# Kernel optimization log

Hardware: AMD Instinct MI355X
Metric: run time of the kernel (lower is better)

The kernel has to match this reference:

```python
import jax, jax.numpy as jnp
import numpy as np

N_NODES = 100000
N_EDGES = 3200000
OUT_CH = 128
X_DIM = 128


def setup_inputs() -> dict:
    key = jax.random.key(0)
    k1, k2, k3, k4 = jax.random.split(key, 4)
    x = jax.random.normal(k1, (N_NODES, X_DIM), dtype=jnp.float32)
    edge_index = jax.random.randint(k2, (2, N_EDGES), 0, N_NODES, dtype=jnp.int64)
    # torch nn.Linear(num_nodes, out_channels): weight [out, N], bias [out]
    W_weight = jax.random.normal(k3, (OUT_CH, N_NODES), dtype=jnp.float32) * (1.0 / np.sqrt(N_NODES))
    W_bias = jax.random.normal(k4, (OUT_CH,), dtype=jnp.float32) * 0.01
    return {"x": x, "edge_index": edge_index, "W_weight": W_weight, "W_bias": W_bias}


def reference(x, edge_index, W_weight, W_bias):
    """LINK forward: logits = A @ W.T + b, A = sparse COO adjacency from edge_index.

    A[r, c] = 1 for each edge (r, c), so row r of the output is
    sum_{c in neighbors(r)} W.T[c] + b  -> gather + segment_sum (SpMM).
    """
    N = x.shape[0]
    row, col = edge_index[0], edge_index[1]
    Wt = W_weight.T  # [N, out]
    gathered = Wt[col]  # [E, out] irregular gather
    logits = jax.ops.segment_sum(gathered, row, num_segments=N) + W_bias  # [N, out]
    return logits
```

## Files before the change

kernel.cpp:

```cpp
#include <hip/hip_runtime.h>
#include <hip/hip_bf16.h>


#define NCHUNK 256
#define RPB 64
#define MAXBUCK 1600
#define CAP 3072
#define SCAN_CHUNK 256

__global__ __launch_bounds__(256) void absmax_kernel(const float* __restrict__ W,
                                                     int n4,
                                                     unsigned int* __restrict__ amax) {
    int i = blockIdx.x * blockDim.x + threadIdx.x;
    int stride = gridDim.x * blockDim.x;
    float m = 0.f;
    const float4* W4 = (const float4*)W;
    for (; i < n4; i += stride) {
        float4 v = W4[i];
        m = fmaxf(m, fmaxf(fmaxf(fabsf(v.x), fabsf(v.y)),
                           fmaxf(fabsf(v.z), fabsf(v.w))));
    }
    for (int off = 32; off > 0; off >>= 1) m = fmaxf(m, __shfl_xor(m, off));
    if ((threadIdx.x & 63) == 0)
        atomicMax(amax, __float_as_uint(m));
}

__global__ __launch_bounds__(256) void quant_kernel(const float* __restrict__ W,
                                                    unsigned char* __restrict__ Wt8,
                                                    const unsigned int* __restrict__ amax,
                                                    int N) {
    __shared__ float tile[128][33];
    int cx = threadIdx.x;
    int oy = threadIdx.y;
    int c = blockIdx.x * 32 + cx;
    for (int k = 0; k < 16; ++k) {
        int o = oy * 16 + k;
        tile[o][cx] = (c < N) ? W[(size_t)o * N + c] : 0.f;
    }
    __syncthreads();
    float M = __uint_as_float(*amax);
    float si = (M > 0.f) ? 127.f / M : 0.f;
    if (c < N) {
        unsigned int w[4];
#pragma unroll
        for (int d = 0; d < 4; ++d) {
            unsigned int acc = 0;
#pragma unroll
            for (int b = 0; b < 4; ++b) {
                int o = oy * 16 + d * 4 + b;
                int qi = __float2int_rn(tile[o][cx] * si) + 128;
                acc |= ((unsigned int)(qi & 0xff)) << (8 * b);
            }
            w[d] = acc;
        }
        *(uint4*)(Wt8 + (size_t)c * 128 + oy * 16) =
            make_uint4(w[0], w[1], w[2], w[3]);
    }
}

__global__ __launch_bounds__(256) void p1_hist(const int* __restrict__ row,
                                               int E, int nbuck,
                                               int* __restrict__ hist) {
    __shared__ int lh[MAXBUCK];
    int b = blockIdx.x;
    for (int k = threadIdx.x; k < nbuck; k += blockDim.x) lh[k] = 0;
    __syncthreads();
    int ch = (E + NCHUNK - 1) / NCHUNK;
    int s = b * ch, e = min(E, s + ch);
    for (int i = s + threadIdx.x; i < e; i += blockDim.x)
        atomicAdd(&lh[row[i] >> 6], 1);
    __syncthreads();
    for (int k = threadIdx.x; k < nbuck; k += blockDim.x)
        hist[k * NCHUNK + b] = lh[k];
}

__global__ void scan_sums(const int* __restrict__ v, int* __restrict__ bsums,
                          int M) {
    __shared__ int s[SCAN_CHUNK];
    int i = blockIdx.x * SCAN_CHUNK + threadIdx.x;
    s[threadIdx.x] = (i < M) ? v[i] : 0;
    __syncthreads();
    for (int off = SCAN_CHUNK / 2; off > 0; off >>= 1) {
        if (threadIdx.x < off) s[threadIdx.x] += s[threadIdx.x + off];
        __syncthreads();
    }
    if (threadIdx.x == 0) bsums[blockIdx.x] = s[0];
}

__global__ __launch_bounds__(256) void scan_offsets_par(int* __restrict__ bsums,
                                                        int nb) {
    __shared__ int s[256];
    __shared__ int carry;
    if (threadIdx.x == 0) carry = 0;
    __syncthreads();
    for (int base = 0; base < nb; base += 256) {
        int i = base + threadIdx.x;
        int v = (i < nb) ? bsums[i] : 0;
        s[threadIdx.x] = v;
        __syncthreads();
        for (int off = 1; off < 256; off <<= 1) {
            int t = (threadIdx.x >= off) ? s[threadIdx.x - off] : 0;
            __syncthreads();
            s[threadIdx.x] += t;
            __syncthreads();
        }
        int incl = s[threadIdx.x];
        int c = carry;
        __syncthreads();
        if (threadIdx.x == 255) carry = c + incl;
        if (i < nb) bsums[i] = c + incl - v;
        __syncthreads();
    }
}

__global__ void scan_final(const int* __restrict__ v,
                           const int* __restrict__ bsums,
                           int* __restrict__ S, int M) {
    __shared__ int s[SCAN_CHUNK];
    int i = blockIdx.x * SCAN_CHUNK + threadIdx.x;
    int x = (i < M) ? v[i] : 0;
    s[threadIdx.x] = x;
    __syncthreads();
    for (int off = 1; off < SCAN_CHUNK; off <<= 1) {
        int t = (threadIdx.x >= off) ? s[threadIdx.x - off] : 0;
        __syncthreads();
        s[threadIdx.x] += t;
        __syncthreads();
    }
    if (i < M) S[i] = bsums[blockIdx.x] + s[threadIdx.x] - x;
}

__global__ __launch_bounds__(256) void p1_scatter(const int* __restrict__ row,
                                                  const int* __restrict__ col,
                                                  int E, int nbuck,
                                                  const int* __restrict__ S,
                                                  unsigned* __restrict__ packed) {
    __shared__ int lc[MAXBUCK];
    int b = blockIdx.x;
    for (int k = threadIdx.x; k < nbuck; k += blockDim.x)
        lc[k] = S[k * NCHUNK + b];
    __syncthreads();
    int ch = (E + NCHUNK - 1) / NCHUNK;
    int s = b * ch, e = min(E, s + ch);
    for (int i = s + threadIdx.x; i < e; i += blockDim.x) {
        int r = row[i], c = col[i];
        int p = atomicAdd(&lc[r >> 6], 1);
        packed[p] = ((unsigned)(r & 63) << 26) | ((unsigned)c << 7);
    }
}

__global__ __launch_bounds__(256) void spmm_fused(
    const unsigned* __restrict__ packed, const int* __restrict__ S,
    const unsigned char* __restrict__ Wt8, const float* __restrict__ bias,
    const unsigned int* __restrict__ amax, float* __restrict__ out, int E,
    int N, int nbuck) {
    __shared__ unsigned g2[CAP];
    __shared__ int rhist[RPB];
    __shared__ int rowstart[RPB + 1];
    __shared__ int cursor[RPB];
    int k = blockIdx.x;
    int start = S[k * NCHUNK];
    int end = (k + 1 < nbuck) ? S[(k + 1) * NCHUNK] : E;
    int cnt = end - start;
    if (cnt > CAP) cnt = CAP;
    if (threadIdx.x < RPB) rhist[threadIdx.x] = 0;
    __syncthreads();
    for (int i = threadIdx.x; i < cnt; i += blockDim.x)
        atomicAdd(&rhist[packed[start + i] >> 26], 1);
    __syncthreads();
    if (threadIdx.x == 0) {
        int acc = 0;
        for (int r = 0; r < RPB; ++r) { rowstart[r] = acc; acc += rhist[r]; }
        rowstart[RPB] = acc;
    }
    __syncthreads();
    if (threadIdx.x < RPB) cursor[threadIdx.x] = rowstart[threadIdx.x];
    __syncthreads();
    for (int i = threadIdx.x; i < cnt; i += blockDim.x) {
        unsigned e2 = packed[start + i];
        int p = atomicAdd(&cursor[e2 >> 26], 1);
        g2[p] = e2 & 0x03FFFFFFu;
    }
    __syncthreads();

    float sg = __uint_as_float(*amax) / 127.f;
    int wave = threadIdx.x >> 6, lane = threadIdx.x & 63;
    int h = lane >> 5;
    int lane4 = (lane & 31) * 4;

    for (int r = wave; r < RPB; r += 4) {
        int gr = k * RPB + r;
        if (gr >= N) break;
        int js = rowstart[r], je = rowstart[r + 1];
        int m = je - js;
        int T = m >> 1;
        unsigned accA = 0, accB = 0;
        int idx = js + h;
        int t = 0;
        for (; t + 4 <= T; t += 4) {
            unsigned e0 = g2[idx + 0];
            unsigned e1 = g2[idx + 2];
            unsigned e2 = g2[idx + 4];
            unsigned e3 = g2[idx + 6];
            idx += 8;
            uint32_t u0 = *(const uint32_t*)(Wt8 + e0 + lane4);
            uint32_t u1 = *(const uint32_t*)(Wt8 + e1 + lane4);
            uint32_t u2 = *(const uint32_t*)(Wt8 + e2 + lane4);
            uint32_t u3 = *(const uint32_t*)(Wt8 + e3 + lane4);
            accA += (u0 & 0x00FF00FFu);
            accB += ((u0 >> 8) & 0x00FF00FFu);
            accA += (u1 & 0x00FF00FFu);
            accB += ((u1 >> 8) & 0x00FF00FFu);
            accA += (u2 & 0x00FF00FFu);
            accB += ((u2 >> 8) & 0x00FF00FFu);
            accA += (u3 & 0x00FF00FFu);
            accB += ((u3 >> 8) & 0x00FF00FFu);
        }
        for (; t < T; ++t) {
            unsigned e0 = g2[idx];
            idx += 2;
            uint32_t u0 = *(const uint32_t*)(Wt8 + e0 + lane4);
            accA += (u0 & 0x00FF00FFu);
            accB += ((u0 >> 8) & 0x00FF00FFu);
        }
        if ((m & 1) && h == 0) {
            unsigned e0 = g2[je - 1];
            uint32_t u0 = *(const uint32_t*)(Wt8 + e0 + lane4);
            accA += (u0 & 0x00FF00FFu);
            accB += ((u0 >> 8) & 0x00FF00FFu);
        }
        accA += __shfl_xor(accA, 32);
        accB += __shfl_xor(accB, 32);
        if (h == 0) {
            float fm = -128.f * (float)m;
            float4 b4 = *(const float4*)(bias + lane4);
            float4 res;
            res.x = fmaf(sg, (float)(accA & 0xffffu) + fm, b4.x);
            res.y = fmaf(sg, (float)(accB & 0xffffu) + fm, b4.y);
            res.z = fmaf(sg, (float)(accA >> 16) + fm, b4.z);
            res.w = fmaf(sg, (float)(accB >> 16) + fm, b4.w);
            *(float4*)(out + (size_t)gr * 128 + lane4) = res;
        }
    }
}

extern "C" void kernel_launch(void* const* d_in, const int* in_sizes, int n_in,
                              void* d_out, int out_size, void* d_ws,
                              size_t ws_size, hipStream_t stream) {
    const int* edge = (const int*)d_in[1];
    const float* W = (const float*)d_in[2];
    const float* bias = (const float*)d_in[3];
    float* out = (float*)d_out;

    const int N = in_sizes[0] / 128;
    const int E = in_sizes[1] / 2;
    const int* row = edge;
    const int* col = edge + E;

    const int nbuck = (N + RPB - 1) / RPB;
    const int M = nbuck * NCHUNK;
    const int nb = (M + SCAN_CHUNK - 1) / SCAN_CHUNK;

    auto align16 = [](size_t v) { return (v + 15) & ~(size_t)15; };
    char* ws = (char*)d_ws;
    size_t off = 0;
    unsigned char* Wt8 = (unsigned char*)(ws + off);
    off = align16(off + (size_t)N * 128);
    unsigned* packed = (unsigned*)(ws + off);
    off = align16(off + (size_t)E * sizeof(unsigned));
    int* hist = (int*)(ws + off);
    off = align16(off + (size_t)M * sizeof(int));
    int* S = (int*)(ws + off);
    off = align16(off + (size_t)M * sizeof(int));
    int* bsums = (int*)(ws + off);
    off = align16(off + (size_t)nb * sizeof(int));
    unsigned int* amax = (unsigned int*)(ws + off);
    off = align16(off + 16);

    hipMemsetAsync(amax, 0, sizeof(unsigned int), stream);

    absmax_kernel<<<1024, 256, 0, stream>>>(W, (128 * N) / 4, amax);
    {
        dim3 block(32, 8);
        dim3 grid((N + 31) / 32);
        quant_kernel<<<grid, block, 0, stream>>>(W, Wt8, amax, N);
    }
    p1_hist<<<NCHUNK, 256, 0, stream>>>(row, E, nbuck, hist);
    scan_sums<<<nb, SCAN_CHUNK, 0, stream>>>(hist, bsums, M);
    scan_offsets_par<<<1, 256, 0, stream>>>(bsums, nb);
    scan_final<<<nb, SCAN_CHUNK, 0, stream>>>(hist, bsums, S, M);
    p1_scatter<<<NCHUNK, 256, 0, stream>>>(row, col, E, nbuck, S, packed);
    spmm_fused<<<nbuck, 256, 0, stream>>>(packed, S, Wt8, bias, amax, out, E, N,
                                          nbuck);
}
```

Baseline: 205.7 us.

## Quadruple bucketing chunks, transpose scan offsets, and use 8-byte gathers in SpMM

Raises the number of histogram/scatter chunks from 256 to 1024 so more blocks run the bucketing phase in parallel. The scan becomes two-level to handle the larger offset array, and it writes a transposed offset table plus a compact per-bucket start array. This makes offset loads coalesced in the scatter and gives the SpMM a direct lookup. The SpMM now splits each wave into four quarter-groups, each loading 8 bytes per edge, with an extra shuffle stage to combine them. The cost is extra scan kernel launches and a hist/offset array four times larger.

```diff
diff --git a/kernel.cpp b/kernel.cpp
--- a/kernel.cpp
+++ b/kernel.cpp
@@ -2,11 +2,10 @@
 #include <hip/hip_bf16.h>
 
 
-#define NCHUNK 256
+#define NCHUNK 1024
 #define RPB 64
 #define MAXBUCK 1600
 #define CAP 3072
-#define SCAN_CHUNK 256
 
 __global__ __launch_bounds__(256) void absmax_kernel(const float* __restrict__ W,
                                                      int n4,
@@ -74,13 +73,13 @@
         hist[k * NCHUNK + b] = lh[k];
 }
 
-__global__ void scan_sums(const int* __restrict__ v, int* __restrict__ bsums,
-                          int M) {
-    __shared__ int s[SCAN_CHUNK];
-    int i = blockIdx.x * SCAN_CHUNK + threadIdx.x;
+__global__ __launch_bounds__(256) void scan_sums(const int* __restrict__ v,
+                                                 int* __restrict__ bsums, int M) {
+    __shared__ int s[256];
+    int i = blockIdx.x * 256 + threadIdx.x;
     s[threadIdx.x] = (i < M) ? v[i] : 0;
     __syncthreads();
-    for (int off = SCAN_CHUNK / 2; off > 0; off >>= 1) {
+    for (int off = 128; off > 0; off >>= 1) {
         if (threadIdx.x < off) s[threadIdx.x] += s[threadIdx.x + off];
         __syncthreads();
     }
@@ -113,32 +112,57 @@
     }
 }
 
-__global__ void scan_final(const int* __restrict__ v,
-                           const int* __restrict__ bsums,
-                           int* __restrict__ S, int M) {
-    __shared__ int s[SCAN_CHUNK];
-    int i = blockIdx.x * SCAN_CHUNK + threadIdx.x;
+__global__ __launch_bounds__(256) void scan_final_inplace(int* __restrict__ v,
+                                                          const int* __restrict__ bsums,
+                                                          int M) {
+    __shared__ int s[256];
+    int i = blockIdx.x * 256 + threadIdx.x;
     int x = (i < M) ? v[i] : 0;
     s[threadIdx.x] = x;
     __syncthreads();
-    for (int off = 1; off < SCAN_CHUNK; off <<= 1) {
+    for (int off = 1; off < 256; off <<= 1) {
         int t = (threadIdx.x >= off) ? s[threadIdx.x - off] : 0;
         __syncthreads();
         s[threadIdx.x] += t;
         __syncthreads();
     }
-    if (i < M) S[i] = bsums[blockIdx.x] + s[threadIdx.x] - x;
+    if (i < M) v[i] = bsums[blockIdx.x] + s[threadIdx.x] - x;
+}
+
+__global__ __launch_bounds__(256) void scan_finalT(const int* __restrict__ hist,
+                                                   const int* __restrict__ bsums,
+                                                   int* __restrict__ S_T,
+                                                   int* __restrict__ bstart,
+                                                   int M, int nbuck) {
+    __shared__ int s[256];
+    int i = blockIdx.x * 256 + threadIdx.x;
+    int x = (i < M) ? hist[i] : 0;
+    s[threadIdx.x] = x;
+    __syncthreads();
+    for (int off = 1; off < 256; off <<= 1) {
+        int t = (threadIdx.x >= off) ? s[threadIdx.x - off] : 0;
+        __syncthreads();
+        s[threadIdx.x] += t;
+        __syncthreads();
+    }
+    if (i < M) {
+        int val = bsums[blockIdx.x] + s[threadIdx.x] - x;
+        int k = i >> 10;
+        int b = i & (NCHUNK - 1);
+        S_T[(size_t)b * nbuck + k] = val;
+        if (b == 0) bstart[k] = val;
+    }
 }
 
 __global__ __launch_bounds__(256) void p1_scatter(const int* __restrict__ row,
                                                   const int* __restrict__ col,
                                                   int E, int nbuck,
-                                                  const int* __restrict__ S,
+                                                  const int* __restrict__ S_T,
                                                   unsigned* __restrict__ packed) {
     __shared__ int lc[MAXBUCK];
     int b = blockIdx.x;
-    for (int k = threadIdx.x; k < nbuck; k += blockDim.x)
-        lc[k] = S[k * NCHUNK + b];
+    const int* Srow = S_T + (size_t)b * nbuck;
+    for (int k = threadIdx.x; k < nbuck; k += blockDim.x) lc[k] = Srow[k];
     __syncthreads();
     int ch = (E + NCHUNK - 1) / NCHUNK;
     int s = b * ch, e = min(E, s + ch);
@@ -150,7 +174,7 @@
 }
 
 __global__ __launch_bounds__(256) void spmm_fused(
-    const unsigned* __restrict__ packed, const int* __restrict__ S,
+    const unsigned* __restrict__ packed, const int* __restrict__ bstart,
     const unsigned char* __restrict__ Wt8, const float* __restrict__ bias,
     const unsigned int* __restrict__ amax, float* __restrict__ out, int E,
     int N, int nbuck) {
@@ -159,8 +183,8 @@
     __shared__ int rowstart[RPB + 1];
     __shared__ int cursor[RPB];
     int k = blockIdx.x;
-    int start = S[k * NCHUNK];
-    int end = (k + 1 < nbuck) ? S[(k + 1) * NCHUNK] : E;
+    int start = bstart[k];
+    int end = (k + 1 < nbuck) ? bstart[k + 1] : E;
     int cnt = end - start;
     if (cnt > CAP) cnt = CAP;
     if (threadIdx.x < RPB) rhist[threadIdx.x] = 0;
@@ -185,61 +209,72 @@
 
     float sg = __uint_as_float(*amax) / 127.f;
     int wave = threadIdx.x >> 6, lane = threadIdx.x & 63;
-    int h = lane >> 5;
-    int lane4 = (lane & 31) * 4;
+    int q = lane >> 4;
+    int sl8 = (lane & 15) * 8;
 
     for (int r = wave; r < RPB; r += 4) {
         int gr = k * RPB + r;
         if (gr >= N) break;
         int js = rowstart[r], je = rowstart[r + 1];
         int m = je - js;
-        int T = m >> 1;
-        unsigned accA = 0, accB = 0;
-        int idx = js + h;
+        unsigned aA0 = 0, aB0 = 0, aA1 = 0, aB1 = 0;
+        int nq = m >> 2;
+        int base = js + q;
         int t = 0;
-        for (; t + 4 <= T; t += 4) {
-            unsigned e0 = g2[idx + 0];
-            unsigned e1 = g2[idx + 2];
-            unsigned e2 = g2[idx + 4];
-            unsigned e3 = g2[idx + 6];
-            idx += 8;
-            uint32_t u0 = *(const uint32_t*)(Wt8 + e0 + lane4);
-            uint32_t u1 = *(const uint32_t*)(Wt8 + e1 + lane4);
-            uint32_t u2 = *(const uint32_t*)(Wt8 + e2 + lane4);
-            uint32_t u3 = *(const uint32_t*)(Wt8 + e3 + lane4);
-            accA += (u0 & 0x00FF00FFu);
-            accB += ((u0 >> 8) & 0x00FF00FFu);
-            accA += (u1 & 0x00FF00FFu);
-            accB += ((u1 >> 8) & 0x00FF00FFu);
-            accA += (u2 & 0x00FF00FFu);
-            accB += ((u2 >> 8) & 0x00FF00FFu);
-            accA += (u3 & 0x00FF00FFu);
-            accB += ((u3 >> 8) & 0x00FF00FFu);
-        }
-        for (; t < T; ++t) {
-            unsigned e0 = g2[idx];
-            idx += 2;
-            uint32_t u0 = *(const uint32_t*)(Wt8 + e0 + lane4);
-            accA += (u0 & 0x00FF00FFu);
-            accB += ((u0 >> 8) & 0x00FF00FFu);
-        }
-        if ((m & 1) && h == 0) {
-            unsigned e0 = g2[je - 1];
-            uint32_t u0 = *(const uint32_t*)(Wt8 + e0 + lane4);
-            accA += (u0 & 0x00FF00FFu);
-            accB += ((u0 >> 8) & 0x00FF00FFu);
-        }
-        accA += __shfl_xor(accA, 32);
-        accB += __shfl_xor(accB, 32);
-        if (h == 0) {
+        for (; t + 2 <= nq; t += 2) {
+            unsigned e0 = g2[base + 4 * t];
+            unsigned e1 = g2[base + 4 * t + 4];
+            uint2 u0 = *(const uint2*)(Wt8 + e0 + sl8);
+            uint2 u1 = *(const uint2*)(Wt8 + e1 + sl8);
+            aA0 += u0.x & 0x00FF00FFu;
+            aB0 += (u0.x >> 8) & 0x00FF00FFu;
+            aA1 += u0.y & 0x00FF00FFu;
+            aB1 += (u0.y >> 8) & 0x00FF00FFu;
+            aA0 += u1.x & 0x00FF00FFu;
+            aB0 += (u1.x >> 8) & 0x00FF00FFu;
+            aA1 += u1.y & 0x00FF00FFu;
+            aB1 += (u1.y >> 8) & 0x00FF00FFu;
+        }
+        if (t < nq) {
+            unsigned e0 = g2[base + 4 * t];
+            uint2 u0 = *(const uint2*)(Wt8 + e0 + sl8);
+            aA0 += u0.x & 0x00FF00FFu;
+            aB0 += (u0.x >> 8) & 0x00FF00FFu;
+            aA1 += u0.y & 0x00FF00FFu;
+            aB1 += (u0.y >> 8) & 0x00FF00FFu;
+        }
+        int rem = m & 3;
+        if (q < rem) {
+            unsigned e0 = g2[js + (nq << 2) + q];
+            uint2 u0 = *(const uint2*)(Wt8 + e0 + sl8);
+            aA0 += u0.x & 0x00FF00FFu;
+            aB0 += (u0.x >> 8) & 0x00FF00FFu;
+            aA1 += u0.y & 0x00FF00FFu;
+            aB1 += (u0.y >> 8) & 0x00FF00FFu;
+        }
+        aA0 += __shfl_xor(aA0, 16);
+        aB0 += __shfl_xor(aB0, 16);
+        aA1 += __shfl_xor(aA1, 16);
+        aB1 += __shfl_xor(aB1, 16);
+        aA0 += __shfl_xor(aA0, 32);
+        aB0 += __shfl_xor(aB0, 32);
+        aA1 += __shfl_xor(aA1, 32);
+        aB1 += __shfl_xor(aB1, 32);
+        if (q == 0) {
             float fm = -128.f * (float)m;
-            float4 b4 = *(const float4*)(bias + lane4);
-            float4 res;
-            res.x = fmaf(sg, (float)(accA & 0xffffu) + fm, b4.x);
-            res.y = fmaf(sg, (float)(accB & 0xffffu) + fm, b4.y);
-            res.z = fmaf(sg, (float)(accA >> 16) + fm, b4.z);
-            res.w = fmaf(sg, (float)(accB >> 16) + fm, b4.w);
-            *(float4*)(out + (size_t)gr * 128 + lane4) = res;
+            float4 b0 = *(const float4*)(bias + sl8);
+            float4 b1 = *(const float4*)(bias + sl8 + 4);
+            float4 r0, r1;
+            r0.x = fmaf(sg, (float)(aA0 & 0xffffu) + fm, b0.x);
+            r0.y = fmaf(sg, (float)(aB0 & 0xffffu) + fm, b0.y);
+            r0.z = fmaf(sg, (float)(aA0 >> 16) + fm, b0.z);
+            r0.w = fmaf(sg, (float)(aB0 >> 16) + fm, b0.w);
+            r1.x = fmaf(sg, (float)(aA1 & 0xffffu) + fm, b1.x);
+            r1.y = fmaf(sg, (float)(aB1 & 0xffffu) + fm, b1.y);
+            r1.z = fmaf(sg, (float)(aA1 >> 16) + fm, b1.z);
+            r1.w = fmaf(sg, (float)(aB1 >> 16) + fm, b1.w);
+            *(float4*)(out + (size_t)gr * 128 + sl8) = r0;
+            *(float4*)(out + (size_t)gr * 128 + sl8 + 4) = r1;
         }
     }
 }
@@ -259,7 +294,8 @@
 
     const int nbuck = (N + RPB - 1) / RPB;
     const int M = nbuck * NCHUNK;
-    const int nb = (M + SCAN_CHUNK - 1) / SCAN_CHUNK;
+    const int nb1 = (M + 255) / 256;
+    const int nb2 = (nb1 + 255) / 256;
 
     auto align16 = [](size_t v) { return (v + 15) & ~(size_t)15; };
     char* ws = (char*)d_ws;
@@ -270,10 +306,14 @@
     off = align16(off + (size_t)E * sizeof(unsigned));
     int* hist = (int*)(ws + off);
     off = align16(off + (size_t)M * sizeof(int));
-    int* S = (int*)(ws + off);
+    int* S_T = (int*)(ws + off);
     off = align16(off + (size_t)M * sizeof(int));
-    int* bsums = (int*)(ws + off);
-    off = align16(off + (size_t)nb * sizeof(int));
+    int* bs1 = (int*)(ws + off);
+    off = align16(off + (size_t)nb1 * sizeof(int));
+    int* bs2 = (int*)(ws + off);
+    off = align16(off + (size_t)nb2 * sizeof(int));
+    int* bstart = (int*)(ws + off);
+    off = align16(off + (size_t)(nbuck + 1) * sizeof(int));
     unsigned int* amax = (unsigned int*)(ws + off);
     off = align16(off + 16);
 
@@ -286,10 +326,12 @@
         quant_kernel<<<grid, block, 0, stream>>>(W, Wt8, amax, N);
     }
     p1_hist<<<NCHUNK, 256, 0, stream>>>(row, E, nbuck, hist);
-    scan_sums<<<nb, SCAN_CHUNK, 0, stream>>>(hist, bsums, M);
-    scan_offsets_par<<<1, 256, 0, stream>>>(bsums, nb);
-    scan_final<<<nb, SCAN_CHUNK, 0, stream>>>(hist, bsums, S, M);
-    p1_scatter<<<NCHUNK, 256, 0, stream>>>(row, col, E, nbuck, S, packed);
-    spmm_fused<<<nbuck, 256, 0, stream>>>(packed, S, Wt8, bias, amax, out, E, N,
-                                          nbuck);
-}
+    scan_sums<<<nb1, 256, 0, stream>>>(hist, bs1, M);
+    scan_sums<<<nb2, 256, 0, stream>>>(bs1, bs2, nb1);
+    scan_offsets_par<<<1, 256, 0, stream>>>(bs2, nb2);
+    scan_final_inplace<<<nb2, 256, 0, stream>>>(bs1, bs2, nb1);
+    scan_finalT<<<nb1, 256, 0, stream>>>(hist, bs1, S_T, bstart, M, nbuck);
+    p1_scatter<<<NCHUNK, 256, 0, stream>>>(row, col, E, nbuck, S_T, packed);
+    spmm_fused<<<nbuck, 256, 0, stream>>>(packed, bstart, Wt8, bias, amax, out,
+                                          E, N, nbuck);
+}
```

After: 230.1 us. 1.12x slower.

## Widen buckets to 128 rows, use 1024-thread blocks, transpose scan offsets

Applied to the files above, without the earlier changes.

Doubles rows per bucket to 128 (782 buckets, fixed as a compile-time constant) and runs the hist, scatter and SpMM kernels with 1024 threads. Scan offsets are written transposed so each scatter block reads a contiguous row, and a separate bucket-start array is emitted. The SpMM kernel keeps edges in registers between the histogram and placement passes, so packed is read only once, and replaces the serial row scan with a parallel scan. The packed format now stores the column directly and shifts it at placement. The hardcoded NB7 ties the code to N=100000. The CAP of 5120 silently drops edges if a bucket ever exceeds it.

```diff
diff --git a/kernel.cpp b/kernel.cpp
--- a/kernel.cpp
+++ b/kernel.cpp
@@ -3,10 +3,9 @@
 
 
 #define NCHUNK 256
-#define RPB 64
-#define MAXBUCK 1600
-#define CAP 3072
-#define SCAN_CHUNK 256
+#define RPB7 128
+#define NB7 782
+#define CAP 5120
 
 __global__ __launch_bounds__(256) void absmax_kernel(const float* __restrict__ W,
                                                      int n4,
@@ -21,8 +20,7 @@
                            fmaxf(fabsf(v.z), fabsf(v.w))));
     }
     for (int off = 32; off > 0; off >>= 1) m = fmaxf(m, __shfl_xor(m, off));
-    if ((threadIdx.x & 63) == 0)
-        atomicMax(amax, __float_as_uint(m));
+    if ((threadIdx.x & 63) == 0) atomicMax(amax, __float_as_uint(m));
 }
 
 __global__ __launch_bounds__(256) void quant_kernel(const float* __restrict__ W,
@@ -58,29 +56,28 @@
     }
 }
 
-__global__ __launch_bounds__(256) void p1_hist(const int* __restrict__ row,
-                                               int E, int nbuck,
-                                               int* __restrict__ hist) {
-    __shared__ int lh[MAXBUCK];
+__global__ __launch_bounds__(1024) void p1_hist(const int* __restrict__ row,
+                                                int E, int* __restrict__ hist) {
+    __shared__ int lh[NB7];
     int b = blockIdx.x;
-    for (int k = threadIdx.x; k < nbuck; k += blockDim.x) lh[k] = 0;
+    for (int k = threadIdx.x; k < NB7; k += blockDim.x) lh[k] = 0;
     __syncthreads();
     int ch = (E + NCHUNK - 1) / NCHUNK;
     int s = b * ch, e = min(E, s + ch);
     for (int i = s + threadIdx.x; i < e; i += blockDim.x)
-        atomicAdd(&lh[row[i] >> 6], 1);
-    __syncthreads();
-    for (int k = threadIdx.x; k < nbuck; k += blockDim.x)
+        atomicAdd(&lh[row[i] >> 7], 1);
+    __syncthreads();
+    for (int k = threadIdx.x; k < NB7; k += blockDim.x)
         hist[k * NCHUNK + b] = lh[k];
 }
 
-__global__ void scan_sums(const int* __restrict__ v, int* __restrict__ bsums,
-                          int M) {
-    __shared__ int s[SCAN_CHUNK];
-    int i = blockIdx.x * SCAN_CHUNK + threadIdx.x;
+__global__ __launch_bounds__(256) void scan_sums(const int* __restrict__ v,
+                                                 int* __restrict__ bsums, int M) {
+    __shared__ int s[256];
+    int i = blockIdx.x * 256 + threadIdx.x;
     s[threadIdx.x] = (i < M) ? v[i] : 0;
     __syncthreads();
-    for (int off = SCAN_CHUNK / 2; off > 0; off >>= 1) {
+    for (int off = 128; off > 0; off >>= 1) {
         if (threadIdx.x < off) s[threadIdx.x] += s[threadIdx.x + off];
         __syncthreads();
     }
@@ -113,85 +110,127 @@
     }
 }
 
-__global__ void scan_final(const int* __restrict__ v,
-                           const int* __restrict__ bsums,
-                           int* __restrict__ S, int M) {
-    __shared__ int s[SCAN_CHUNK];
-    int i = blockIdx.x * SCAN_CHUNK + threadIdx.x;
-    int x = (i < M) ? v[i] : 0;
+__global__ __launch_bounds__(256) void scan_finalT(const int* __restrict__ hist,
+                                                   const int* __restrict__ bsums,
+                                                   int* __restrict__ S_T,
+                                                   int* __restrict__ bstart,
+                                                   int M) {
+    __shared__ int s[256];
+    int i = blockIdx.x * 256 + threadIdx.x;
+    int x = (i < M) ? hist[i] : 0;
     s[threadIdx.x] = x;
     __syncthreads();
-    for (int off = 1; off < SCAN_CHUNK; off <<= 1) {
+    for (int off = 1; off < 256; off <<= 1) {
         int t = (threadIdx.x >= off) ? s[threadIdx.x - off] : 0;
         __syncthreads();
         s[threadIdx.x] += t;
         __syncthreads();
     }
-    if (i < M) S[i] = bsums[blockIdx.x] + s[threadIdx.x] - x;
-}
-
-__global__ __launch_bounds__(256) void p1_scatter(const int* __restrict__ row,
-                                                  const int* __restrict__ col,
-                                                  int E, int nbuck,
-                                                  const int* __restrict__ S,
-                                                  unsigned* __restrict__ packed) {
-    __shared__ int lc[MAXBUCK];
+    if (i < M) {
+        int val = bsums[blockIdx.x] + s[threadIdx.x] - x;
+        int k = i >> 8;
+        int b = i & (NCHUNK - 1);
+        S_T[(size_t)b * NB7 + k] = val;
+        if (b == 0) bstart[k] = val;
+    }
+}
+
+__global__ __launch_bounds__(1024) void p1_scatter(const int* __restrict__ row,
+                                                   const int* __restrict__ col,
+                                                   int E,
+                                                   const int* __restrict__ S_T,
+                                                   unsigned* __restrict__ packed) {
+    __shared__ int lc[NB7];
     int b = blockIdx.x;
-    for (int k = threadIdx.x; k < nbuck; k += blockDim.x)
-        lc[k] = S[k * NCHUNK + b];
+    const int* Srow = S_T + (size_t)b * NB7;
+    for (int k = threadIdx.x; k < NB7; k += blockDim.x) lc[k] = Srow[k];
     __syncthreads();
     int ch = (E + NCHUNK - 1) / NCHUNK;
     int s = b * ch, e = min(E, s + ch);
     for (int i = s + threadIdx.x; i < e; i += blockDim.x) {
         int r = row[i], c = col[i];
-        int p = atomicAdd(&lc[r >> 6], 1);
-        packed[p] = ((unsigned)(r & 63) << 26) | ((unsigned)c << 7);
-    }
-}
-
-__global__ __launch_bounds__(256) void spmm_fused(
-    const unsigned* __restrict__ packed, const int* __restrict__ S,
+        int p = atomicAdd(&lc[r >> 7], 1);
+        packed[p] = ((unsigned)(r & 127) << 17) | (unsigned)c;
+    }
+}
+
+__global__ __launch_bounds__(1024) void spmm_fused(
+    const unsigned* __restrict__ packed, const int* __restrict__ bstart,
     const unsigned char* __restrict__ Wt8, const float* __restrict__ bias,
     const unsigned int* __restrict__ amax, float* __restrict__ out, int E,
-    int N, int nbuck) {
+    int N) {
     __shared__ unsigned g2[CAP];
-    __shared__ int rhist[RPB];
-    __shared__ int rowstart[RPB + 1];
-    __shared__ int cursor[RPB];
+    __shared__ int rhist[RPB7];
+    __shared__ int rs[RPB7 + 1];
+    __shared__ int cursor[RPB7];
+    __shared__ int sscan[RPB7];
     int k = blockIdx.x;
-    int start = S[k * NCHUNK];
-    int end = (k + 1 < nbuck) ? S[(k + 1) * NCHUNK] : E;
+    int start = bstart[k];
+    int end = (k + 1 < NB7) ? bstart[k + 1] : E;
     int cnt = end - start;
     if (cnt > CAP) cnt = CAP;
-    if (threadIdx.x < RPB) rhist[threadIdx.x] = 0;
-    __syncthreads();
-    for (int i = threadIdx.x; i < cnt; i += blockDim.x)
-        atomicAdd(&rhist[packed[start + i] >> 26], 1);
-    __syncthreads();
-    if (threadIdx.x == 0) {
-        int acc = 0;
-        for (int r = 0; r < RPB; ++r) { rowstart[r] = acc; acc += rhist[r]; }
-        rowstart[RPB] = acc;
-    }
-    __syncthreads();
-    if (threadIdx.x < RPB) cursor[threadIdx.x] = rowstart[threadIdx.x];
-    __syncthreads();
-    for (int i = threadIdx.x; i < cnt; i += blockDim.x) {
-        unsigned e2 = packed[start + i];
-        int p = atomicAdd(&cursor[e2 >> 26], 1);
-        g2[p] = e2 & 0x03FFFFFFu;
+
+    int tid = threadIdx.x;
+    if (tid < RPB7) rhist[tid] = 0;
+    __syncthreads();
+
+    unsigned st0 = 0, st1 = 0, st2 = 0, st3 = 0, st4 = 0;
+    {
+        int i;
+        i = tid;
+        if (i < cnt) { st0 = packed[start + i]; atomicAdd(&rhist[st0 >> 17], 1); }
+        i = tid + 1024;
+        if (i < cnt) { st1 = packed[start + i]; atomicAdd(&rhist[st1 >> 17], 1); }
+        i = tid + 2048;
+        if (i < cnt) { st2 = packed[start + i]; atomicAdd(&rhist[st2 >> 17], 1); }
+        i = tid + 3072;
+        if (i < cnt) { st3 = packed[start + i]; atomicAdd(&rhist[st3 >> 17], 1); }
+        i = tid + 4096;
+        if (i < cnt) { st4 = packed[start + i]; atomicAdd(&rhist[st4 >> 17], 1); }
+    }
+    __syncthreads();
+    {
+        int v = 0;
+        if (tid < RPB7) { v = rhist[tid]; sscan[tid] = v; }
+        __syncthreads();
+        for (int off = 1; off < RPB7; off <<= 1) {
+            int t = 0;
+            if (tid < RPB7 && tid >= off) t = sscan[tid - off];
+            __syncthreads();
+            if (tid < RPB7 && tid >= off) sscan[tid] += t;
+            __syncthreads();
+        }
+        if (tid < RPB7) {
+            rs[tid] = sscan[tid] - v;
+            cursor[tid] = sscan[tid] - v;
+            if (tid == RPB7 - 1) rs[RPB7] = sscan[RPB7 - 1];
+        }
+    }
+    __syncthreads();
+    {
+        int i;
+        i = tid;
+        if (i < cnt) { int p = atomicAdd(&cursor[st0 >> 17], 1); g2[p] = (st0 & 0x1FFFFu) << 7; }
+        i = tid + 1024;
+        if (i < cnt) { int p = atomicAdd(&cursor[st1 >> 17], 1); g2[p] = (st1 & 0x1FFFFu) << 7; }
+        i = tid + 2048;
+        if (i < cnt) { int p = atomicAdd(&cursor[st2 >> 17], 1); g2[p] = (st2 & 0x1FFFFu) << 7; }
+        i = tid + 3072;
+        if (i < cnt) { int p = atomicAdd(&cursor[st3 >> 17], 1); g2[p] = (st3 & 0x1FFFFu) << 7; }
+        i = tid + 4096;
+        if (i < cnt) { int p = atomicAdd(&cursor[st4 >> 17], 1); g2[p] = (st4 & 0x1FFFFu) << 7; }
     }
     __syncthreads();
 
     float sg = __uint_as_float(*amax) / 127.f;
-    int wave = threadIdx.x >> 6, lane = threadIdx.x & 63;
+    int wave = tid >> 6, lane = tid & 63;
     int h = lane >> 5;
     int lane4 = (lane & 31) * 4;
 
-    for (int r = wave; r < RPB; r += 4) {
-        int gr = k * RPB + r;
-        if (gr >= N) break;
-        int js = rowstart[r], je = rowstart[r + 1];
+    for (int ri = 0; ri < 8; ++ri) {
+        int r = wave * 8 + ri;
+        int gr = k * RPB7 + r;
+        int js = rs[r], je = rs[r + 1];
         int m = je - js;
         int T = m >> 1;
         unsigned accA = 0, accB = 0;
@@ -231,7 +270,7 @@
         }
         accA += __shfl_xor(accA, 32);
         accB += __shfl_xor(accB, 32);
-        if (h == 0) {
+        if (h == 0 && gr < N) {
             float fm = -128.f * (float)m;
             float4 b4 = *(const float4*)(bias + lane4);
             float4 res;
@@ -257,9 +296,8 @@
     const int* row = edge;
     const int* col = edge + E;
 
-    const int nbuck = (N + RPB - 1) / RPB;
-    const int M = nbuck * NCHUNK;
-    const int nb = (M + SCAN_CHUNK - 1) / SCAN_CHUNK;
+    const int M = NB7 * NCHUNK;
+    const int nb1 = (M + 255) / 256;
 
     auto align16 = [](size_t v) { return (v + 15) & ~(size_t)15; };
     char* ws = (char*)d_ws;
@@ -270,10 +308,12 @@
     off = align16(off + (size_t)E * sizeof(unsigned));
     int* hist = (int*)(ws + off);
     off = align16(off + (size_t)M * sizeof(int));
-    int* S = (int*)(ws + off);
+    int* S_T = (int*)(ws + off);
     off = align16(off + (size_t)M * sizeof(int));
-    int* bsums = (int*)(ws + off);
-    off = align16(off + (size_t)nb * sizeof(int));
+    int* bs1 = (int*)(ws + off);
+    off = align16(off + (size_t)nb1 * sizeof(int));
+    int* bstart = (int*)(ws + off);
+    off = align16(off + (size_t)(NB7 + 1) * sizeof(int));
     unsigned int* amax = (unsigned int*)(ws + off);
     off = align16(off + 16);
 
@@ -285,11 +325,11 @@
         dim3 grid((N + 31) / 32);
         quant_kernel<<<grid, block, 0, stream>>>(W, Wt8, amax, N);
     }
-    p1_hist<<<NCHUNK, 256, 0, stream>>>(row, E, nbuck, hist);
-    scan_sums<<<nb, SCAN_CHUNK, 0, stream>>>(hist, bsums, M);
-    scan_offsets_par<<<1, 256, 0, stream>>>(bsums, nb);
-    scan_final<<<nb, SCAN_CHUNK, 0, stream>>>(hist, bsums, S, M);
-    p1_scatter<<<NCHUNK, 256, 0, stream>>>(row, col, E, nbuck, S, packed);
-    spmm_fused<<<nbuck, 256, 0, stream>>>(packed, S, Wt8, bias, amax, out, E, N,
-                                          nbuck);
-}
+    p1_hist<<<NCHUNK, 1024, 0, stream>>>(row, E, hist);
+    scan_sums<<<nb1, 256, 0, stream>>>(hist, bs1, M);
+    scan_offsets_par<<<1, 256, 0, stream>>>(bs1, nb1);
+    scan_finalT<<<nb1, 256, 0, stream>>>(hist, bs1, S_T, bstart, M);
+    p1_scatter<<<NCHUNK, 1024, 0, stream>>>(row, col, E, S_T, packed);
+    spmm_fused<<<NB7, 1024, 0, stream>>>(packed, bstart, Wt8, bias, amax, out,
+                                         E, N);
+}
```

Result: faster. 189.5 us (-7.8%).

## Replace global histogram/scan/scatter with per-chunk LDS sort and run-gather in SpMM

Applied to the files above, without the earlier changes.

Five preprocessing kernels (histogram, three-pass global scan, scatter) are replaced by a single sortchunk kernel. Each 1024-thread block buckets its 12.5K-edge chunk in LDS and writes the sorted chunk plus per-bucket offset/length run info. The SpMM kernel then scans the 256 run lengths for its bucket and gathers the runs from every chunk into LDS before the per-row sort. This removes launch overhead and the global scan passes, and makes the scatter writes coalesced. In exchange, each SpMM block does 256 small serial per-thread run copies, and the 14-bit length and 17-bit column packing limits hold only for these sizes.

```diff
diff --git a/kernel.cpp b/kernel.cpp
--- a/kernel.cpp
+++ b/kernel.cpp
@@ -1,12 +1,10 @@
 #include <hip/hip_runtime.h>
-#include <hip/hip_bf16.h>
 
 
 #define NCHUNK 256
-#define RPB 64
-#define MAXBUCK 1600
+#define STRIDE 13312
+#define MAXB 1600
 #define CAP 3072
-#define SCAN_CHUNK 256
 
 __global__ __launch_bounds__(256) void absmax_kernel(const float* __restrict__ W,
                                                      int n4,
@@ -21,8 +19,7 @@
                            fmaxf(fabsf(v.z), fabsf(v.w))));
     }
     for (int off = 32; off > 0; off >>= 1) m = fmaxf(m, __shfl_xor(m, off));
-    if ((threadIdx.x & 63) == 0)
-        atomicMax(amax, __float_as_uint(m));
+    if ((threadIdx.x & 63) == 0) atomicMax(amax, __float_as_uint(m));
 }
 
 __global__ __launch_bounds__(256) void quant_kernel(const float* __restrict__ W,
@@ -58,140 +55,149 @@
     }
 }
 
-__global__ __launch_bounds__(256) void p1_hist(const int* __restrict__ row,
-                                               int E, int nbuck,
-                                               int* __restrict__ hist) {
-    __shared__ int lh[MAXBUCK];
-    int b = blockIdx.x;
-    for (int k = threadIdx.x; k < nbuck; k += blockDim.x) lh[k] = 0;
-    __syncthreads();
-    int ch = (E + NCHUNK - 1) / NCHUNK;
-    int s = b * ch, e = min(E, s + ch);
-    for (int i = s + threadIdx.x; i < e; i += blockDim.x)
-        atomicAdd(&lh[row[i] >> 6], 1);
-    __syncthreads();
-    for (int k = threadIdx.x; k < nbuck; k += blockDim.x)
-        hist[k * NCHUNK + b] = lh[k];
-}
-
-__global__ void scan_sums(const int* __restrict__ v, int* __restrict__ bsums,
-                          int M) {
-    __shared__ int s[SCAN_CHUNK];
-    int i = blockIdx.x * SCAN_CHUNK + threadIdx.x;
-    s[threadIdx.x] = (i < M) ? v[i] : 0;
-    __syncthreads();
-    for (int off = SCAN_CHUNK / 2; off > 0; off >>= 1) {
-        if (threadIdx.x < off) s[threadIdx.x] += s[threadIdx.x + off];
-        __syncthreads();
-    }
-    if (threadIdx.x == 0) bsums[blockIdx.x] = s[0];
-}
-
-__global__ __launch_bounds__(256) void scan_offsets_par(int* __restrict__ bsums,
-                                                        int nb) {
-    __shared__ int s[256];
-    __shared__ int carry;
-    if (threadIdx.x == 0) carry = 0;
-    __syncthreads();
-    for (int base = 0; base < nb; base += 256) {
-        int i = base + threadIdx.x;
-        int v = (i < nb) ? bsums[i] : 0;
-        s[threadIdx.x] = v;
-        __syncthreads();
-        for (int off = 1; off < 256; off <<= 1) {
-            int t = (threadIdx.x >= off) ? s[threadIdx.x - off] : 0;
-            __syncthreads();
-            s[threadIdx.x] += t;
-            __syncthreads();
-        }
-        int incl = s[threadIdx.x];
-        int c = carry;
-        __syncthreads();
-        if (threadIdx.x == 255) carry = c + incl;
-        if (i < nb) bsums[i] = c + incl - v;
-        __syncthreads();
-    }
-}
-
-__global__ void scan_final(const int* __restrict__ v,
-                           const int* __restrict__ bsums,
-                           int* __restrict__ S, int M) {
-    __shared__ int s[SCAN_CHUNK];
-    int i = blockIdx.x * SCAN_CHUNK + threadIdx.x;
-    int x = (i < M) ? v[i] : 0;
-    s[threadIdx.x] = x;
-    __syncthreads();
-    for (int off = 1; off < SCAN_CHUNK; off <<= 1) {
-        int t = (threadIdx.x >= off) ? s[threadIdx.x - off] : 0;
-        __syncthreads();
-        s[threadIdx.x] += t;
-        __syncthreads();
-    }
-    if (i < M) S[i] = bsums[blockIdx.x] + s[threadIdx.x] - x;
-}
-
-__global__ __launch_bounds__(256) void p1_scatter(const int* __restrict__ row,
+__global__ __launch_bounds__(1024) void sortchunk(const int* __restrict__ row,
                                                   const int* __restrict__ col,
-                                                  int E, int nbuck,
-                                                  const int* __restrict__ S,
-                                                  unsigned* __restrict__ packed) {
-    __shared__ int lc[MAXBUCK];
-    int b = blockIdx.x;
-    for (int k = threadIdx.x; k < nbuck; k += blockDim.x)
-        lc[k] = S[k * NCHUNK + b];
-    __syncthreads();
-    int ch = (E + NCHUNK - 1) / NCHUNK;
-    int s = b * ch, e = min(E, s + ch);
-    for (int i = s + threadIdx.x; i < e; i += blockDim.x) {
-        int r = row[i], c = col[i];
-        int p = atomicAdd(&lc[r >> 6], 1);
-        packed[p] = ((unsigned)(r & 63) << 26) | ((unsigned)c << 7);
-    }
+                                                  int E, int chr_, int nbuck,
+                                                  unsigned* __restrict__ packed,
+                                                  unsigned* __restrict__ runinfo) {
+    __shared__ unsigned g2[STRIDE];
+    __shared__ int lh[MAXB];
+    __shared__ int ls[MAXB];
+    __shared__ int cur[MAXB];
+    __shared__ int part[512];
+    int c = blockIdx.x, tid = threadIdx.x;
+    int s = c * chr_;
+    int e = min(E, s + chr_);
+    int cnt = e - s;
+    for (int k = tid; k < nbuck; k += 1024) lh[k] = 0;
+    __syncthreads();
+    int rst[13], cst[13];
+#pragma unroll
+    for (int j = 0; j < 13; ++j) {
+        int i = j * 1024 + tid;
+        rst[j] = -1;
+        cst[j] = 0;
+        if (i < cnt) {
+            rst[j] = row[s + i];
+            cst[j] = col[s + i];
+            atomicAdd(&lh[rst[j] >> 6], 1);
+        }
+    }
+    __syncthreads();
+    int v0 = 0, v1 = 0, v2 = 0, v3 = 0, mysum = 0;
+    if (tid < 512) {
+        int b4 = tid * 4;
+        v0 = (b4 + 0 < nbuck) ? lh[b4 + 0] : 0;
+        v1 = (b4 + 1 < nbuck) ? lh[b4 + 1] : 0;
+        v2 = (b4 + 2 < nbuck) ? lh[b4 + 2] : 0;
+        v3 = (b4 + 3 < nbuck) ? lh[b4 + 3] : 0;
+        mysum = v0 + v1 + v2 + v3;
+        part[tid] = mysum;
+    }
+    __syncthreads();
+    for (int off = 1; off < 512; off <<= 1) {
+        int t = 0;
+        if (tid < 512 && tid >= off) t = part[tid - off];
+        __syncthreads();
+        if (tid < 512) part[tid] += t;
+        __syncthreads();
+    }
+    if (tid < 512) {
+        int excl = part[tid] - mysum;
+        int b4 = tid * 4;
+        if (b4 + 0 < nbuck) ls[b4 + 0] = excl;
+        if (b4 + 1 < nbuck) ls[b4 + 1] = excl + v0;
+        if (b4 + 2 < nbuck) ls[b4 + 2] = excl + v0 + v1;
+        if (b4 + 3 < nbuck) ls[b4 + 3] = excl + v0 + v1 + v2;
+    }
+    __syncthreads();
+    for (int k = tid; k < nbuck; k += 1024) cur[k] = ls[k];
+    __syncthreads();
+#pragma unroll
+    for (int j = 0; j < 13; ++j) {
+        if (rst[j] >= 0) {
+            int p = atomicAdd(&cur[rst[j] >> 6], 1);
+            g2[p] = ((unsigned)(rst[j] & 63) << 17) | (unsigned)cst[j];
+        }
+    }
+    __syncthreads();
+#pragma unroll
+    for (int j = 0; j < 13; ++j) {
+        int i = j * 1024 + tid;
+        if (i < cnt) packed[(size_t)c * STRIDE + i] = g2[i];
+    }
+    for (int k = tid; k < nbuck; k += 1024)
+        runinfo[(size_t)c * nbuck + k] =
+            ((unsigned)ls[k] << 14) | (unsigned)lh[k];
 }
 
 __global__ __launch_bounds__(256) void spmm_fused(
-    const unsigned* __restrict__ packed, const int* __restrict__ S,
+    const unsigned* __restrict__ packed, const unsigned* __restrict__ runinfo,
     const unsigned char* __restrict__ Wt8, const float* __restrict__ bias,
-    const unsigned int* __restrict__ amax, float* __restrict__ out, int E,
-    int N, int nbuck) {
+    const unsigned int* __restrict__ amax, float* __restrict__ out, int N,
+    int nbuck) {
+    __shared__ unsigned stage[CAP];
     __shared__ unsigned g2[CAP];
-    __shared__ int rhist[RPB];
-    __shared__ int rowstart[RPB + 1];
-    __shared__ int cursor[RPB];
-    int k = blockIdx.x;
-    int start = S[k * NCHUNK];
-    int end = (k + 1 < nbuck) ? S[(k + 1) * NCHUNK] : E;
-    int cnt = end - start;
-    if (cnt > CAP) cnt = CAP;
-    if (threadIdx.x < RPB) rhist[threadIdx.x] = 0;
-    __syncthreads();
-    for (int i = threadIdx.x; i < cnt; i += blockDim.x)
-        atomicAdd(&rhist[packed[start + i] >> 26], 1);
-    __syncthreads();
-    if (threadIdx.x == 0) {
-        int acc = 0;
-        for (int r = 0; r < RPB; ++r) { rowstart[r] = acc; acc += rhist[r]; }
-        rowstart[RPB] = acc;
-    }
-    __syncthreads();
-    if (threadIdx.x < RPB) cursor[threadIdx.x] = rowstart[threadIdx.x];
-    __syncthreads();
-    for (int i = threadIdx.x; i < cnt; i += blockDim.x) {
-        unsigned e2 = packed[start + i];
-        int p = atomicAdd(&cursor[e2 >> 26], 1);
-        g2[p] = e2 & 0x03FFFFFFu;
+    __shared__ int lensc[256];
+    __shared__ int rhist[64];
+    __shared__ int rs[65];
+    __shared__ int cur[64];
+    __shared__ int sc2[64];
+    __shared__ int tot;
+    int k = blockIdx.x, tid = threadIdx.x;
+    unsigned ri = runinfo[(size_t)tid * nbuck + k];
+    int len = ri & 0x3FFFu;
+    int loc = ri >> 14;
+    lensc[tid] = len;
+    __syncthreads();
+    for (int off = 1; off < 256; off <<= 1) {
+        int t = (tid >= off) ? lensc[tid - off] : 0;
+        __syncthreads();
+        lensc[tid] += t;
+        __syncthreads();
+    }
+    int dst = lensc[tid] - len;
+    if (tid == 255) tot = lensc[255];
+    __syncthreads();
+    int cnt = min(tot, CAP);
+    const unsigned* srcp = packed + (size_t)tid * STRIDE + loc;
+    for (int j = 0; j < len; ++j)
+        if (dst + j < CAP) stage[dst + j] = srcp[j];
+    if (tid < 64) rhist[tid] = 0;
+    __syncthreads();
+    for (int i = tid; i < cnt; i += 256) atomicAdd(&rhist[stage[i] >> 17], 1);
+    __syncthreads();
+    if (tid < 64) sc2[tid] = rhist[tid];
+    __syncthreads();
+    for (int off = 1; off < 64; off <<= 1) {
+        int t = 0;
+        if (tid < 64 && tid >= off) t = sc2[tid - off];
+        __syncthreads();
+        if (tid < 64) sc2[tid] += t;
+        __syncthreads();
+    }
+    if (tid < 64) {
+        rs[tid] = sc2[tid] - rhist[tid];
+        cur[tid] = rs[tid];
+        if (tid == 63) rs[64] = sc2[63];
+    }
+    __syncthreads();
+    for (int i = tid; i < cnt; i += 256) {
+        unsigned v = stage[i];
+        int p = atomicAdd(&cur[v >> 17], 1);
+        g2[p] = (v & 0x1FFFFu) << 7;
     }
     __syncthreads();
 
     float sg = __uint_as_float(*amax) / 127.f;
-    int wave = threadIdx.x >> 6, lane = threadIdx.x & 63;
+    int wave = tid >> 6, lane = tid & 63;
     int h = lane >> 5;
     int lane4 = (lane & 31) * 4;
 
-    for (int r = wave; r < RPB; r += 4) {
-        int gr = k * RPB + r;
+    for (int r = wave; r < 64; r += 4) {
+        int gr = k * 64 + r;
         if (gr >= N) break;
-        int js = rowstart[r], je = rowstart[r + 1];
+        int js = rs[r], je = rs[r + 1];
         int m = je - js;
         int T = m >> 1;
         unsigned accA = 0, accB = 0;
@@ -257,9 +263,8 @@
     const int* row = edge;
     const int* col = edge + E;
 
-    const int nbuck = (N + RPB - 1) / RPB;
-    const int M = nbuck * NCHUNK;
-    const int nb = (M + SCAN_CHUNK - 1) / SCAN_CHUNK;
+    const int nbuck = (N + 63) / 64;
+    const int chr_ = (E + NCHUNK - 1) / NCHUNK;
 
     auto align16 = [](size_t v) { return (v + 15) & ~(size_t)15; };
     char* ws = (char*)d_ws;
@@ -267,13 +272,9 @@
     unsigned char* Wt8 = (unsigned char*)(ws + off);
     off = align16(off + (size_t)N * 128);
     unsigned* packed = (unsigned*)(ws + off);
-    off = align16(off + (size_t)E * sizeof(unsigned));
-    int* hist = (int*)(ws + off);
-    off = align16(off + (size_t)M * sizeof(int));
-    int* S = (int*)(ws + off);
-    off = align16(off + (size_t)M * sizeof(int));
-    int* bsums = (int*)(ws + off);
-    off = align16(off + (size_t)nb * sizeof(int));
+    off = align16(off + (size_t)NCHUNK * STRIDE * sizeof(unsigned));
+    unsigned* runinfo = (unsigned*)(ws + off);
+    off = align16(off + (size_t)NCHUNK * nbuck * sizeof(unsigned));
     unsigned int* amax = (unsigned int*)(ws + off);
     off = align16(off + 16);
 
@@ -285,11 +286,8 @@
         dim3 grid((N + 31) / 32);
         quant_kernel<<<grid, block, 0, stream>>>(W, Wt8, amax, N);
     }
-    p1_hist<<<NCHUNK, 256, 0, stream>>>(row, E, nbuck, hist);
-    scan_sums<<<nb, SCAN_CHUNK, 0, stream>>>(hist, bsums, M);
-    scan_offsets_par<<<1, 256, 0, stream>>>(bsums, nb);
-    scan_final<<<nb, SCAN_CHUNK, 0, stream>>>(hist, bsums, S, M);
-    p1_scatter<<<NCHUNK, 256, 0, stream>>>(row, col, E, nbuck, S, packed);
-    spmm_fused<<<nbuck, 256, 0, stream>>>(packed, S, Wt8, bias, amax, out, E, N,
-                                          nbuck);
-}
+    sortchunk<<<NCHUNK, 1024, 0, stream>>>(row, col, E, chr_, nbuck, packed,
+                                           runinfo);
+    spmm_fused<<<nbuck, 256, 0, stream>>>(packed, runinfo, Wt8, bias, amax, out,
+                                          N, nbuck);
+}
```

After: 193.4 us. 6.0% less time.
